# Performance work log

Measured on AMD Instinct MI355X. Metric: run time of the kernel, lower is better.

## Reference

```python
import jax, jax.numpy as jnp
import numpy as np

SR = 44100
N_FFT = 2048
N_BINS = 64
HOP = 512
POWER = 2.0
FREQ_BINS = N_FFT // 2 + 1  # 1025
BATCH = 32
LEN_AUDIO = 441000  # 10 seconds at 44.1 kHz


def _fourier_kernels():
    # Periodic (fftbins=True) Hann window, matching scipy.signal.get_window('hann', n_fft)
    n = np.arange(N_FFT)
    window = 0.5 - 0.5 * np.cos(2.0 * np.pi * n / N_FFT)
    k = np.arange(FREQ_BINS)[:, None]  # [freq_bins, 1]
    phase = 2.0 * np.pi * k * n[None, :] / N_FFT  # [freq_bins, n_fft]
    wsin = (np.sin(phase) * window[None, :]).astype(np.float32)[:, None, :]  # [F,1,n_fft]
    wcos = (np.cos(phase) * window[None, :]).astype(np.float32)[:, None, :]
    return jnp.asarray(wsin), jnp.asarray(wcos)


def setup_inputs() -> dict:
    key = jax.random.key(0)
    k1, k2 = jax.random.split(key)
    x = jax.random.normal(k1, (BATCH, 1, LEN_AUDIO), dtype=jnp.float32)
    wsin, wcos = _fourier_kernels()
    # Gammatone filterbank matrix [n_bins, freq_bins]; treated as a fixed parameter.
    gammatone_basis = jax.random.uniform(k2, (N_BINS, FREQ_BINS), dtype=jnp.float32) * 0.01
    return {"x": x, "wsin": wsin, "wcos": wcos, "gammatone_basis": gammatone_basis}


def _conv1d(x, w, stride):
    # x: [B, 1, L], w: [F, 1, K] -> [B, F, T]
    return jax.lax.conv_general_dilated(
        x, w, window_strides=(stride,), padding='VALID',
        dimension_numbers=('NCH', 'OIH', 'NCH'))


def reference(x, wsin, wcos, gammatone_basis):
    pad = N_FFT // 2
    xp = jnp.pad(x, ((0, 0), (0, 0), (pad, pad)), mode='reflect')
    s = _conv1d(xp, wsin, HOP)
    c = _conv1d(xp, wcos, HOP)
    spec = jnp.sqrt(s * s + c * c) ** POWER  # [B, F, T]
    # [n_bins, F] @ [B, F, T] -> [B, n_bins, T]
    return jnp.einsum('nf,bft->bnt', gammatone_basis, spec)
```

## Files before the change

kernel.cpp:

```cpp
#include <hip/hip_runtime.h>
#include <stdint.h>

typedef __attribute__((ext_vector_type(4))) float f32x4;
typedef __attribute__((ext_vector_type(8))) short bf16x8;
typedef __attribute__((ext_vector_type(8))) unsigned short u16x8;
typedef __attribute__((ext_vector_type(2))) unsigned int u32x2;

#define B_SZ   32
#define L_AUD  441000
#define PAD_A  1024
#define LP     443048
#define T_FR   862
#define J_TOT  27584
#define JPAD   27648
#define F_BINS 1025
#define NFFT   2048
#define NB     64
#define FPAD   1152
#define NT_J   108
#define NT_F   9
#define NWG    (NT_J * NT_F)
#define ROWB   886096

#define W2_OFF     0
#define W2_BYTES   (NT_F * 32 * 16384)
#define GB2_OFF    W2_BYTES
#define GB2_BYTES  (NB * FPAD * 2)
#define UB_OFF     (GB2_OFF + GB2_BYTES)
#define UB_BYTES   ((size_t)JPAD * 2048 * 2)
#define WS_FOLD    (UB_OFF + UB_BYTES)
#define SLAB_BYTES ((size_t)NT_F * NB * JPAD * 4)
#define WS_FOLD_SLAB (WS_FOLD + SLAB_BYTES)

#define FB_XBP_OFF   0
#define FB_XBP_BYTES (B_SZ * LP * 2)
#define FB_WBT_OFF   FB_XBP_BYTES
#define FB_WBT_BYTES (NT_F * 32 * 2 * 16384)
#define FB_GB_OFF    (FB_WBT_OFF + FB_WBT_BYTES)
#define FB_WS_NEED   (FB_GB_OFF + GB2_BYTES)
#define FB_SLAB_OFF  FB_WS_NEED
#define FB_WS_BIG    ((size_t)FB_SLAB_OFF + SLAB_BYTES)

__device__ __forceinline__ uint16_t f2bf(float f) {
  union { float f; uint32_t u; } c; c.f = f;
  uint32_t r = c.u + 0x7FFFu + ((c.u >> 16) & 1u);
  return (uint16_t)(r >> 16);
}
__device__ __forceinline__ float bf2f(uint32_t u) {
  union { uint32_t u; float f; } c; c.u = u << 16; return c.f;
}

__device__ __forceinline__ f32x4 mfma16(bf16x8 a, bf16x8 b, f32x4 c) {
  return __builtin_amdgcn_mfma_f32_16x16x32_bf16(a, b, c, 0, 0, 0);
}

#define GLD16(g, l) __builtin_amdgcn_global_load_lds( \
    (__attribute__((address_space(1))) void*)(g),     \
    (__attribute__((address_space(3))) void*)(l), 16, 0, 0)

__device__ __forceinline__ int refl(int p) {
  int s = p - PAD_A;
  s = s < 0 ? -s : s;
  s = s >= L_AUD ? (2 * L_AUD - 2 - s) : s;
  return s;
}


__global__ __launch_bounds__(256) void build_gb(const float* __restrict__ g,
                                                uint16_t* __restrict__ gb) {
  int i = blockIdx.x * 256 + threadIdx.x;
  int n = i / FPAD;
  int f = i - n * FPAD;
  gb[i] = f2bf(f < F_BINS ? g[n * F_BINS + f] : 0.0f);
}

__global__ __launch_bounds__(256) void reduce9(const float* __restrict__ slab,
                                               float* __restrict__ out) {
  int i = blockIdx.x * 256 + threadIdx.x;
  if (i >= J_TOT * NB) return;
  int b = i / (NB * T_FR);
  int rem = i - b * (NB * T_FR);
  int n = rem / T_FR;
  int t = rem - n * T_FR;
  int j = b * T_FR + t;
  float s = 0.f;
#pragma unroll
  for (int fb = 0; fb < NT_F; ++fb)
    s += slab[((size_t)fb * NB + n) * JPAD + j];
  out[i] = s;
}


__global__ __launch_bounds__(256) void build_wbt2(const float* __restrict__ wsin,
                                                  const float* __restrict__ wcos,
                                                  uint16_t* __restrict__ wbt) {
  int idx = blockIdx.x * 256 + threadIdx.x;
  int e = idx & 7;
  int s = (idx >> 3) & 7;
  int jp = (idx >> 6) & 127;
  int kkt = (idx >> 13) & 31;
  int fb = idx >> 18;
  int v = s ^ (jp & 7);
  int r = jp * 2 + (v >> 2);
  int k = (v & 3) * 8 + e;
  int plane = r >> 7;
  int f = fb * 128 + (r & 127);
  int m = kkt * 32 + k;
  float val = 0.f;
  if (f < F_BINS) {
    int mm = (m == 0) ? 1024 : m;
    val = plane ? wsin[(size_t)f * NFFT + mm] : wcos[(size_t)f * NFFT + mm];
  }
  wbt[idx] = f2bf(val);
}

__global__ __launch_bounds__(128) void build_ub(const float* __restrict__ x,
                                                uint16_t* __restrict__ ub) {
  __shared__ float xs[2048];
  int jg = blockIdx.x;
  int tid = threadIdx.x;
  uint16_t* outp = ub + (size_t)jg * 2048;
  if (jg >= J_TOT) {
    u16x8 z = (u16x8)0;
    *(u16x8*)(outp + tid * 8) = z;
    *(u16x8*)(outp + 1024 + tid * 8) = z;
    return;
  }
  int b = jg / T_FR, t = jg - b * T_FR;
  int c = t * 512;
  const float* xb = x + (size_t)b * L_AUD;
  if (t >= 2 && t <= 859) {
    const float4* src = (const float4*)(xb + c - PAD_A);
    float4* dl = (float4*)xs;
#pragma unroll
    for (int i = 0; i < 4; ++i) dl[tid * 4 + i] = src[tid * 4 + i];
  } else {
#pragma unroll
    for (int i = 0; i < 16; ++i) xs[tid * 16 + i] = xb[refl(c + tid * 16 + i)];
  }
  __syncthreads();
  int m0 = tid * 8;
  u16x8 vp, vm;
#pragma unroll
  for (int i = 0; i < 8; ++i) {
    int m = m0 + i;
    if (m == 0) { vp[i] = f2bf(xs[1024]); vm[i] = 0; }
    else {
      float a = xs[m], r = xs[2048 - m];
      vp[i] = f2bf(a + r);
      vm[i] = f2bf(a - r);
    }
  }
  *(u16x8*)(outp + m0) = vp;
  *(u16x8*)(outp + 1024 + m0) = vm;
}

template <bool USE_SLAB>
__global__ __launch_bounds__(512, 2) void gammatone_fold(
    const char* __restrict__ ub, const char* __restrict__ wbt2,
    const char* __restrict__ gb, float* __restrict__ dst) {
  __shared__ __align__(16) char smem[147456];

  const int tid = threadIdx.x;
  const int w = tid >> 6, l = tid & 63;
  const int lgrp = l >> 4, l15 = l & 15;
  const int plane = w >> 2;
  const int rw = (w >> 1) & 1;
  const int jw = w & 1;

  const int orig = blockIdx.x;
  const int xcd = orig & 7, slot = orig >> 3;
  const int q = NWG / 8, r = NWG & 7;
  const int wkid = (xcd < r ? xcd * (q + 1) : r * (q + 1) + (xcd - r) * q) + slot;
  const int jb = wkid / NT_F;
  const int fb = wkid - jb * NT_F;
  const int j0 = jb * 256;
  const int f0 = fb * 128;

  const int ssn = w >> 2, q4 = w & 3;
  const int aoff_sta = w * 2048 + l * 16;
  const int boff_sta = 16384 + ssn * 16384 + q4 * 4096 + l * 16;
  const int vsw = (l & 7) ^ (l >> 3);
  const char* bsrc[4];
#pragma unroll
  for (int i = 0; i < 4; ++i) {
    int col = j0 + q4 * 64 + i * 16 + (l >> 3) * 2 + (vsw >> 2);
    bsrc[i] = ub + (size_t)col * 4096 + ssn * 2048 + (vsw & 3) * 16;
  }
  const char* wbtA = wbt2 + (size_t)fb * 524288;

#define STAGEF(kkt, off) do {                                               \
    const char* ga_ = wbtA + (size_t)(kkt) * 16384 + aoff_sta;              \
    GLD16(ga_,        smem + (off) + aoff_sta);                             \
    GLD16(ga_ + 1024, smem + (off) + aoff_sta + 1024);                      \
    GLD16(bsrc[0] + (size_t)(kkt) * 64, smem + (off) + boff_sta);           \
    GLD16(bsrc[1] + (size_t)(kkt) * 64, smem + (off) + boff_sta + 1024);    \
    GLD16(bsrc[2] + (size_t)(kkt) * 64, smem + (off) + boff_sta + 2048);    \
    GLD16(bsrc[3] + (size_t)(kkt) * 64, smem + (off) + boff_sta + 3072);    \
  } while (0)

  const int slb = ((lgrp | ((l15 & 1) << 2)) ^ (l15 >> 1)) << 4;
  int aoff[4], bvo[8];
#pragma unroll
  for (int m = 0; m < 4; ++m)
    aoff[m] = (plane * 64 + rw * 32 + m * 8 + (l15 >> 1)) * 128 + slb;
#pragma unroll
  for (int n = 0; n < 8; ++n)
    bvo[n] = 16384 + plane * 16384 + (jw * 64 + n * 8 + (l15 >> 1)) * 128 + slb;

  STAGEF(0, 0);
  STAGEF(1, 49152);
  asm volatile("s_waitcnt vmcnt(6)" ::: "memory");
  asm volatile("s_barrier" ::: "memory");

  f32x4 acc[4][8];
#pragma unroll
  for (int m = 0; m < 4; ++m)
#pragma unroll
    for (int n = 0; n < 8; ++n) acc[m][n] = (f32x4){0.f, 0.f, 0.f, 0.f};

  unsigned b0 = 0, b1 = 49152, b2 = 98304;
  for (int kk = 0; kk < 32; ++kk) {
    bf16x8 av[4], bv[8];
#pragma unroll
    for (int m = 0; m < 4; ++m) av[m] = *(const bf16x8*)(smem + b0 + aoff[m]);
#pragma unroll
    for (int n = 0; n < 8; ++n) bv[n] = *(const bf16x8*)(smem + b0 + bvo[n]);
    if (kk < 30) STAGEF(kk + 2, b2);
    __builtin_amdgcn_s_setprio(1);
#pragma unroll
    for (int m = 0; m < 4; ++m)
#pragma unroll
      for (int n = 0; n < 8; ++n)
        acc[m][n] = mfma16(av[m], bv[n], acc[m][n]);
    __builtin_amdgcn_s_setprio(0);
    if (kk < 30)       asm volatile("s_waitcnt vmcnt(6)" ::: "memory");
    else if (kk == 30) asm volatile("s_waitcnt vmcnt(0)" ::: "memory");
    asm volatile("s_barrier" ::: "memory");
    unsigned t = b0; b0 = b1; b1 = b2; b2 = t;
  }

  __syncthreads();
  if (plane == 0) {
#pragma unroll
    for (int m = 0; m < 4; ++m) {
      int fi = rw * 64 + m * 16 + lgrp * 4;
#pragma unroll
      for (int n = 0; n < 8; ++n) {
        int j = jw * 128 + n * 16 + l15;
        f32x4 c = acc[m][n];
        uint32_t lo = (uint32_t)f2bf(c.x * c.x) |
                      ((uint32_t)f2bf(c.y * c.y) << 16);
        uint32_t hi = (uint32_t)f2bf(c.z * c.z) |
                      ((uint32_t)f2bf(c.w * c.w) << 16);
        int off = j * 256 + ((fi * 2) ^ ((j & 7) << 4));
        *(u32x2*)(smem + off) = (u32x2){lo, hi};
      }
    }
  }
  __syncthreads();
  if (plane == 1) {
#pragma unroll
    for (int m = 0; m < 4; ++m) {
      int fi = rw * 64 + m * 16 + lgrp * 4;
#pragma unroll
      for (int n = 0; n < 8; ++n) {
        int j = jw * 128 + n * 16 + l15;
        int off = j * 256 + ((fi * 2) ^ ((j & 7) << 4));
        u32x2 v = *(u32x2*)(smem + off);
        f32x4 s = acc[m][n];
        uint32_t lo = (uint32_t)f2bf(bf2f(v.x & 0xffffu) + s.x * s.x) |
                      ((uint32_t)f2bf(bf2f(v.x >> 16) + s.y * s.y) << 16);
        uint32_t hi = (uint32_t)f2bf(bf2f(v.y & 0xffffu) + s.z * s.z) |
                      ((uint32_t)f2bf(bf2f(v.y >> 16) + s.w * s.w) << 16);
        *(u32x2*)(smem + off) = (u32x2){lo, hi};
      }
    }
  }
  __syncthreads();

  f32x4 acc2[4][2];
#pragma unroll
  for (int m = 0; m < 4; ++m) {
    acc2[m][0] = (f32x4){0.f, 0.f, 0.f, 0.f};
    acc2[m][1] = (f32x4){0.f, 0.f, 0.f, 0.f};
  }
  const int jwq = w * 32;
#pragma unroll
  for (int ks = 0; ks < 4; ++ks) {
    bf16x8 gf[4], sf[2];
#pragma unroll
    for (int m2 = 0; m2 < 4; ++m2) {
      int grow = m2 * 16 + l15;
      gf[m2] = *(const bf16x8*)(gb + ((size_t)grow * FPAD + f0 + ks * 32 + lgrp * 8) * 2);
    }
#pragma unroll
    for (int nf = 0; nf < 2; ++nf) {
      int j = jwq + nf * 16 + l15;
      sf[nf] = *(const bf16x8*)(smem + j * 256 + (((ks * 32 + lgrp * 8) * 2) ^ ((j & 7) << 4)));
    }
#pragma unroll
    for (int m2 = 0; m2 < 4; ++m2)
#pragma unroll
      for (int nf = 0; nf < 2; ++nf)
        acc2[m2][nf] = mfma16(gf[m2], sf[nf], acc2[m2][nf]);
  }

#pragma unroll
  for (int nf = 0; nf < 2; ++nf) {
    int jg = j0 + jwq + nf * 16 + l15;
    if (USE_SLAB) {
      float* sl = dst + ((size_t)fb * NB) * JPAD + jg;
#pragma unroll
      for (int m2 = 0; m2 < 4; ++m2)
#pragma unroll
        for (int r2 = 0; r2 < 4; ++r2) {
          int nout = m2 * 16 + lgrp * 4 + r2;
          sl[(size_t)nout * JPAD] = acc2[m2][nf][r2];
        }
    } else if (jg < J_TOT) {
      int b = jg / T_FR;
      int t = jg - b * T_FR;
      float* ob = dst + (size_t)(b * NB) * T_FR + t;
#pragma unroll
      for (int m2 = 0; m2 < 4; ++m2)
#pragma unroll
        for (int r2 = 0; r2 < 4; ++r2) {
          int nout = m2 * 16 + lgrp * 4 + r2;
          atomicAdd(ob + (size_t)nout * T_FR, acc2[m2][nf][r2]);
        }
    }
  }
}


__global__ __launch_bounds__(256) void build_xbp(const float* __restrict__ x,
                                                 uint16_t* __restrict__ xbp) {
  int i = blockIdx.x * 256 + threadIdx.x;
  int b = i / LP;
  int p = i - b * LP;
  xbp[i] = f2bf(x[b * L_AUD + refl(p)]);
}

__global__ __launch_bounds__(256) void build_wbtf(const float* __restrict__ wsin,
                                                  const float* __restrict__ wcos,
                                                  uint16_t* __restrict__ wbt) {
  int idx = blockIdx.x * 256 + threadIdx.x;
  int e = idx & 7;
  int l = (idx >> 3) & 63;
  int s = (idx >> 9) & 1;
  int fm = (idx >> 10) & 15;
  int kkt = (idx >> 14) & 31;
  int fb = idx >> 19;
  int tr = fm * 16 + (l & 15);
  int k = kkt * 64 + s * 32 + ((l >> 4) << 3) + e;
  int plane = (tr >> 6) & 1;
  int f = fb * 128 + ((tr >> 7) << 6) + (tr & 63);
  float v = (f < F_BINS) ? (plane ? wcos[f * NFFT + k] : wsin[f * NFFT + k]) : 0.0f;
  wbt[idx] = f2bf(v);
}

__device__ __forceinline__ void load_a2(bf16x8 (&d)[2][2], const char* p) {
  d[0][0] = *(const bf16x8*)(p);
  d[0][1] = *(const bf16x8*)(p + 1024);
  d[1][0] = *(const bf16x8*)(p + 2048);
  d[1][1] = *(const bf16x8*)(p + 3072);
}
__device__ __forceinline__ void load_b4(bf16x8 (&dst)[4][2], const char* p,
                                        int k0, int k1) {
#pragma unroll
  for (int n = 0; n < 4; ++n) {
    dst[n][0] = *(const bf16x8*)(p + n * 2048 + k0);
    dst[n][1] = *(const bf16x8*)(p + n * 2048 + k1);
  }
}
__device__ __forceinline__ void mfma_pair(f32x4 (*ac)[4],
                                          const bf16x8 (&av)[2][2],
                                          const bf16x8 (&bv)[4][2]) {
#pragma unroll
  for (int m = 0; m < 2; ++m)
#pragma unroll
    for (int n = 0; n < 4; ++n) {
      ac[m][n] = mfma16(av[m][0], bv[n][0], ac[m][n]);
      ac[m][n] = mfma16(av[m][1], bv[n][1], ac[m][n]);
    }
}

template <bool USE_SLAB>
__global__ __launch_bounds__(512, 2) void gammatone_fb(
    const char* __restrict__ xbp, const char* __restrict__ wbt,
    const char* __restrict__ gb, float* __restrict__ dst) {
  __shared__ __align__(16) char smem[65536];

  const int tid = threadIdx.x;
  const int w = tid >> 6, l = tid & 63;
  const int lgrp = l >> 4, l15 = l & 15;
  const int wr = w >> 2, wc = w & 3;

  const int orig = blockIdx.y * NT_J + blockIdx.x;
  const int xcd = orig & 7, slot = orig >> 3;
  const int q = NWG / 8, r = NWG & 7;
  const int wkid = (xcd < r ? xcd * (q + 1) : r * (q + 1) + (xcd - r) * q) + slot;
  const int fb = wkid / NT_J;
  const int jb = wkid - fb * NT_J;
  const int j0 = jb * 256;
  const int f0 = fb * 128;

  const int xr = (((tid & 7) << 4)) ^ ((((tid >> 3) & 7)) << 4);
  size_t fbase[2][2];
#pragma unroll
  for (int h = 0; h < 2; ++h)
#pragma unroll
    for (int i = 0; i < 2; ++i) {
      int col = j0 + h * 128 + i * 64 + (tid >> 3);
      if (col > J_TOT - 1) col = J_TOT - 1;
      int b = col / T_FR;
      int t = col - b * T_FR;
      fbase[h][i] = (size_t)b * ROWB + (size_t)t * 1024 + (size_t)xr;
    }

#define STAGE_B2(kkt, buf) do {                                             \
    char* d0_ = smem + (buf) * 32768;                                       \
    char* d1_ = smem + (buf) * 32768 + 16384;                               \
    GLD16(xbp + fbase[0][0] + (size_t)(kkt) * 128, d0_ + w * 1024 + l * 16);\
    GLD16(xbp + fbase[0][1] + (size_t)(kkt) * 128, d0_ + 8192 + w * 1024 + l * 16);\
    GLD16(xbp + fbase[1][0] + (size_t)(kkt) * 128, d1_ + w * 1024 + l * 16);\
    GLD16(xbp + fbase[1][1] + (size_t)(kkt) * 128, d1_ + 8192 + w * 1024 + l * 16);\
  } while (0)

  const int albase = l15 * 128;
  const int xa = (l15 & 7) << 4;
  const int k0 = (lgrp * 16) ^ xa;
  const int k1 = (64 + lgrp * 16) ^ xa;
  const int jrb = (wc & 1) * 64;
  const char* Bb0 = smem + (wc >> 1) * 16384 + jrb * 128 + albase;
  const char* Bb1 = Bb0 + 32768;
  const char* wbt_a = wbt + (size_t)fb * 32 * 32768 + wr * 16384 + (size_t)l * 16;

  STAGE_B2(0, 0);
  STAGE_B2(1, 1);
  asm volatile("s_waitcnt vmcnt(0)" ::: "memory");
  __builtin_amdgcn_s_barrier();

  f32x4 acc[8][4];
#pragma unroll
  for (int m = 0; m < 8; ++m)
#pragma unroll
    for (int n = 0; n < 4; ++n) acc[m][n] = (f32x4){0.f, 0.f, 0.f, 0.f};

  bf16x8 bvA[4][2], bvB[4][2], av0[2][2], av1[2][2];
  load_b4(bvA, Bb0, k0, k1);
  load_a2(av0, wbt_a);
  asm volatile("s_waitcnt lgkmcnt(0)" ::: "memory");
  __builtin_amdgcn_s_barrier();

#define SP1 __builtin_amdgcn_s_setprio(1)
#define SP0 __builtin_amdgcn_s_setprio(0)

#define TILEFB(KK, bvC, bvN, BbN, STG, NXT) do {                            \
    const char* aT = wbt_a + (size_t)(KK) * 32768;                          \
    if (STG) STAGE_B2((KK) + 2, (KK) & 1);                                  \
    load_a2(av1, aT + 2 * 2048);                                            \
    SP1; mfma_pair(&acc[0], av0, bvC); SP0;                                 \
    load_a2(av0, aT + 4 * 2048);                                            \
    SP1; mfma_pair(&acc[2], av1, bvC); SP0;                                 \
    load_a2(av1, aT + 6 * 2048);                                            \
    if (NXT) load_b4(bvN, BbN, k0, k1);                                     \
    SP1; mfma_pair(&acc[4], av0, bvC); SP0;                                 \
    if (NXT) load_a2(av0, wbt_a + (size_t)((KK) + 1) * 32768);              \
    SP1; mfma_pair(&acc[6], av1, bvC); SP0;                                 \
    asm volatile("s_waitcnt lgkmcnt(0)" ::: "memory");                      \
    __builtin_amdgcn_s_barrier();                                           \
  } while (0)

  for (int kk = 0; kk < 30; kk += 2) {
    TILEFB(kk,     bvA, bvB, Bb1, 1, 1);
    TILEFB(kk + 1, bvB, bvA, Bb0, 1, 1);
  }
  TILEFB(30, bvA, bvB, Bb1, 0, 1);
  TILEFB(31, bvB, bvA, Bb0, 0, 0);

  __syncthreads();
#pragma unroll
  for (int m = 0; m < 4; ++m) {
    int fi = wr * 64 + m * 16 + lgrp * 4;
#pragma unroll
    for (int n = 0; n < 4; ++n) {
      int j = wc * 64 + n * 16 + l15;
      f32x4 s = acc[m][n], c = acc[m + 4][n];
      uint32_t lo = (uint32_t)f2bf(s.x * s.x + c.x * c.x) |
                    ((uint32_t)f2bf(s.y * s.y + c.y * c.y) << 16);
      uint32_t hi = (uint32_t)f2bf(s.z * s.z + c.z * c.z) |
                    ((uint32_t)f2bf(s.w * s.w + c.w * c.w) << 16);
      int off = j * 256 + ((fi * 2) ^ ((j & 7) << 4));
      *(u32x2*)(smem + off) = (u32x2){lo, hi};
    }
  }
  __syncthreads();

  f32x4 acc2[4][2];
#pragma unroll
  for (int m = 0; m < 4; ++m) {
    acc2[m][0] = (f32x4){0.f, 0.f, 0.f, 0.f};
    acc2[m][1] = (f32x4){0.f, 0.f, 0.f, 0.f};
  }
  const int jw = w * 32;
#pragma unroll
  for (int ks = 0; ks < 4; ++ks) {
    bf16x8 gf[4], sf[2];
#pragma unroll
    for (int m2 = 0; m2 < 4; ++m2) {
      int grow = m2 * 16 + l15;
      gf[m2] = *(const bf16x8*)(gb + ((size_t)grow * FPAD + f0 + ks * 32 + lgrp * 8) * 2);
    }
#pragma unroll
    for (int nf = 0; nf < 2; ++nf) {
      int j = jw + nf * 16 + l15;
      sf[nf] = *(const bf16x8*)(smem + j * 256 + (((ks * 32 + lgrp * 8) * 2) ^ ((j & 7) << 4)));
    }
#pragma unroll
    for (int m2 = 0; m2 < 4; ++m2)
#pragma unroll
      for (int nf = 0; nf < 2; ++nf)
        acc2[m2][nf] = mfma16(gf[m2], sf[nf], acc2[m2][nf]);
  }

#pragma unroll
  for (int nf = 0; nf < 2; ++nf) {
    int jg = j0 + jw + nf * 16 + l15;
    if (USE_SLAB) {
      float* sl = dst + ((size_t)fb * NB) * JPAD + jg;
#pragma unroll
      for (int m2 = 0; m2 < 4; ++m2)
#pragma unroll
        for (int r2 = 0; r2 < 4; ++r2) {
          int nout = m2 * 16 + lgrp * 4 + r2;
          sl[(size_t)nout * JPAD] = acc2[m2][nf][r2];
        }
    } else if (jg < J_TOT) {
      int b = jg / T_FR;
      int t = jg - b * T_FR;
      float* ob = dst + (size_t)(b * NB) * T_FR + t;
#pragma unroll
      for (int m2 = 0; m2 < 4; ++m2)
#pragma unroll
        for (int r2 = 0; r2 < 4; ++r2) {
          int nout = m2 * 16 + lgrp * 4 + r2;
          atomicAdd(ob + (size_t)nout * T_FR, acc2[m2][nf][r2]);
        }
    }
  }
}

extern "C" void kernel_launch(void* const* d_in, const int* in_sizes, int n_in,
                              void* d_out, int out_size, void* d_ws, size_t ws_size,
                              hipStream_t stream) {
  (void)in_sizes; (void)n_in;
  const float* x    = (const float*)d_in[0];
  const float* wsin = (const float*)d_in[1];
  const float* wcos = (const float*)d_in[2];
  const float* g    = (const float*)d_in[3];
  char* ws = (char*)d_ws;

  if (ws_size >= (size_t)WS_FOLD) {
    uint16_t* wbt2 = (uint16_t*)(ws + W2_OFF);
    uint16_t* gbp  = (uint16_t*)(ws + GB2_OFF);
    uint16_t* ub   = (uint16_t*)(ws + UB_OFF);
    build_wbt2<<<(W2_BYTES / 2) / 256, 256, 0, stream>>>(wsin, wcos, wbt2);
    build_gb<<<(NB * FPAD) / 256, 256, 0, stream>>>(g, gbp);
    build_ub<<<JPAD, 128, 0, stream>>>(x, ub);
    if (ws_size >= (size_t)WS_FOLD_SLAB) {
      float* slab = (float*)(ws + WS_FOLD);
      gammatone_fold<true><<<NWG, 512, 0, stream>>>(
          (const char*)ub, (const char*)wbt2, (const char*)gbp, slab);
      reduce9<<<(J_TOT * NB + 255) / 256, 256, 0, stream>>>(slab, (float*)d_out);
    } else {
      hipMemsetAsync(d_out, 0, (size_t)out_size * sizeof(float), stream);
      gammatone_fold<false><<<NWG, 512, 0, stream>>>(
          (const char*)ub, (const char*)wbt2, (const char*)gbp, (float*)d_out);
    }
    return;
  }

  if (ws_size < (size_t)FB_WS_NEED) return;
  uint16_t* xbp = (uint16_t*)(ws + FB_XBP_OFF);
  uint16_t* wbt = (uint16_t*)(ws + FB_WBT_OFF);
  uint16_t* gbp = (uint16_t*)(ws + FB_GB_OFF);
  build_xbp<<<(B_SZ * LP) / 256, 256, 0, stream>>>(x, xbp);
  build_wbtf<<<(FB_WBT_BYTES / 2) / 256, 256, 0, stream>>>(wsin, wcos, wbt);
  build_gb<<<(NB * FPAD) / 256, 256, 0, stream>>>(g, gbp);
  if (ws_size >= (size_t)FB_WS_BIG) {
    float* slab = (float*)(ws + FB_SLAB_OFF);
    gammatone_fb<true><<<dim3(NT_J, NT_F), 512, 0, stream>>>(
        (const char*)xbp, (const char*)wbt, (const char*)gbp, slab);
    reduce9<<<(J_TOT * NB + 255) / 256, 256, 0, stream>>>(slab, (float*)d_out);
  } else {
    hipMemsetAsync(d_out, 0, (size_t)out_size * sizeof(float), stream);
    gammatone_fb<false><<<dim3(NT_J, NT_F), 512, 0, stream>>>(
        (const char*)xbp, (const char*)wbt, (const char*)gbp, (float*)d_out);
  }
}
```

Baseline: 218.4 us.

## Pre-swizzle operands into MFMA fragment layout and load directly to registers

The A (windowed Fourier) and B (folded audio frame) operands are now stored in global memory already arranged in the MFMA fragment order. The main GEMM loop can then read them straight into registers with double-buffered global loads, with no LDS staging and no barriers. The j-tile is halved to 128, which doubles the workgroup count and shrinks shared memory to 32KB. In exchange, each workgroup loses the LDS reuse of operands across waves, so more global/L2 traffic is needed, and latency hiding relies only on the register prefetch.

```diff
diff --git a/kernel.cpp b/kernel.cpp
--- a/kernel.cpp
+++ b/kernel.cpp
@@ -17,9 +17,9 @@
 #define NFFT   2048
 #define NB     64
 #define FPAD   1152
-#define NT_J   108
 #define NT_F   9
-#define NWG    (NT_J * NT_F)
+#define NT_J2  216
+#define NWG2   (NT_J2 * NT_F)
 #define ROWB   886096
 
 #define W2_OFF     0
@@ -40,6 +40,8 @@
 #define FB_WS_NEED   (FB_GB_OFF + GB2_BYTES)
 #define FB_SLAB_OFF  FB_WS_NEED
 #define FB_WS_BIG    ((size_t)FB_SLAB_OFF + SLAB_BYTES)
+#define FB_NT_J      108
+#define FB_NWG       (FB_NT_J * NT_F)
 
 __device__ __forceinline__ uint16_t f2bf(float f) {
   union { float f; uint32_t u; } c; c.f = f;
@@ -91,39 +93,39 @@
 }
 
 
-__global__ __launch_bounds__(256) void build_wbt2(const float* __restrict__ wsin,
+__global__ __launch_bounds__(256) void build_wbt3(const float* __restrict__ wsin,
                                                   const float* __restrict__ wcos,
                                                   uint16_t* __restrict__ wbt) {
   int idx = blockIdx.x * 256 + threadIdx.x;
   int e = idx & 7;
-  int s = (idx >> 3) & 7;
-  int jp = (idx >> 6) & 127;
+  int lane = (idx >> 3) & 63;
+  int fm = (idx >> 9) & 15;
   int kkt = (idx >> 13) & 31;
   int fb = idx >> 18;
-  int v = s ^ (jp & 7);
-  int r = jp * 2 + (v >> 2);
-  int k = (v & 3) * 8 + e;
-  int plane = r >> 7;
-  int f = fb * 128 + (r & 127);
-  int m = kkt * 32 + k;
+  int row = fm * 16 + (lane & 15);
+  int k = kkt * 32 + ((lane >> 4) << 3) + e;
+  int plane = row >> 7;
+  int f = fb * 128 + (row & 127);
   float val = 0.f;
   if (f < F_BINS) {
-    int mm = (m == 0) ? 1024 : m;
+    int mm = (k == 0) ? 1024 : k;
     val = plane ? wsin[(size_t)f * NFFT + mm] : wcos[(size_t)f * NFFT + mm];
   }
   wbt[idx] = f2bf(val);
 }
 
-__global__ __launch_bounds__(128) void build_ub(const float* __restrict__ x,
-                                                uint16_t* __restrict__ ub) {
+__global__ __launch_bounds__(128) void build_ubf(const float* __restrict__ x,
+                                                 uint16_t* __restrict__ ub) {
   __shared__ float xs[2048];
   int jg = blockIdx.x;
   int tid = threadIdx.x;
-  uint16_t* outp = ub + (size_t)jg * 2048;
+  int m0 = tid * 8;
+  size_t basef = (((size_t)(jg >> 4) * 32 + (m0 >> 5)) * 2) * 1024 +
+                 (size_t)((((m0 >> 3) & 3) * 16 + (jg & 15)) * 16);
   if (jg >= J_TOT) {
     u16x8 z = (u16x8)0;
-    *(u16x8*)(outp + tid * 8) = z;
-    *(u16x8*)(outp + 1024 + tid * 8) = z;
+    *(u16x8*)((char*)ub + basef) = z;
+    *(u16x8*)((char*)ub + basef + 1024) = z;
     return;
   }
   int b = jg / T_FR, t = jg - b * T_FR;
@@ -139,7 +141,6 @@
     for (int i = 0; i < 16; ++i) xs[tid * 16 + i] = xb[refl(c + tid * 16 + i)];
   }
   __syncthreads();
-  int m0 = tid * 8;
   u16x8 vp, vm;
 #pragma unroll
   for (int i = 0; i < 8; ++i) {
@@ -151,15 +152,18 @@
       vm[i] = f2bf(a - r);
     }
   }
-  *(u16x8*)(outp + m0) = vp;
-  *(u16x8*)(outp + 1024 + m0) = vm;
-}
+  *(u16x8*)((char*)ub + basef) = vp;
+  *(u16x8*)((char*)ub + basef + 1024) = vm;
+}
+
+#define SP1 __builtin_amdgcn_s_setprio(1)
+#define SP0 __builtin_amdgcn_s_setprio(0)
 
 template <bool USE_SLAB>
-__global__ __launch_bounds__(512, 2) void gammatone_fold(
-    const char* __restrict__ ub, const char* __restrict__ wbt2,
+__global__ __launch_bounds__(512, 2) void gammatone_fold2(
+    const char* __restrict__ ubf, const char* __restrict__ wbt3,
     const char* __restrict__ gb, float* __restrict__ dst) {
-  __shared__ __align__(16) char smem[147456];
+  __shared__ __align__(16) char smem[32768];
 
   const int tid = threadIdx.x;
   const int w = tid >> 6, l = tid & 63;
@@ -169,76 +173,57 @@
   const int jw = w & 1;
 
   const int orig = blockIdx.x;
-  const int xcd = orig & 7, slot = orig >> 3;
-  const int q = NWG / 8, r = NWG & 7;
-  const int wkid = (xcd < r ? xcd * (q + 1) : r * (q + 1) + (xcd - r) * q) + slot;
+  const int wkid = (orig & 7) * 243 + (orig >> 3);
   const int jb = wkid / NT_F;
   const int fb = wkid - jb * NT_F;
-  const int j0 = jb * 256;
+  const int j0 = jb * 128;
   const int f0 = fb * 128;
 
-  const int ssn = w >> 2, q4 = w & 3;
-  const int aoff_sta = w * 2048 + l * 16;
-  const int boff_sta = 16384 + ssn * 16384 + q4 * 4096 + l * 16;
-  const int vsw = (l & 7) ^ (l >> 3);
-  const char* bsrc[4];
-#pragma unroll
-  for (int i = 0; i < 4; ++i) {
-    int col = j0 + q4 * 64 + i * 16 + (l >> 3) * 2 + (vsw >> 2);
-    bsrc[i] = ub + (size_t)col * 4096 + ssn * 2048 + (vsw & 3) * 16;
-  }
-  const char* wbtA = wbt2 + (size_t)fb * 524288;
-
-#define STAGEF(kkt, off) do {                                               \
-    const char* ga_ = wbtA + (size_t)(kkt) * 16384 + aoff_sta;              \
-    GLD16(ga_,        smem + (off) + aoff_sta);                             \
-    GLD16(ga_ + 1024, smem + (off) + aoff_sta + 1024);                      \
-    GLD16(bsrc[0] + (size_t)(kkt) * 64, smem + (off) + boff_sta);           \
-    GLD16(bsrc[1] + (size_t)(kkt) * 64, smem + (off) + boff_sta + 1024);    \
-    GLD16(bsrc[2] + (size_t)(kkt) * 64, smem + (off) + boff_sta + 2048);    \
-    GLD16(bsrc[3] + (size_t)(kkt) * 64, smem + (off) + boff_sta + 3072);    \
+  const char* aB = wbt3 + (((size_t)fb * 32) * 16 + plane * 8 + rw * 4) * 1024
+                        + (size_t)l * 16;
+  const char* bB = ubf + (((size_t)(jb * 8 + jw * 4) * 32) * 2 + plane) * 1024
+                       + (size_t)l * 16;
+
+#define LOADT(kkt, av_, bv_) do {                                           \
+    const char* a_ = aB + (size_t)(kkt) * 16384;                            \
+    const char* b_ = bB + (size_t)(kkt) * 2048;                             \
+    av_[0] = *(const bf16x8*)(a_);                                          \
+    av_[1] = *(const bf16x8*)(a_ + 1024);                                   \
+    av_[2] = *(const bf16x8*)(a_ + 2048);                                   \
+    av_[3] = *(const bf16x8*)(a_ + 3072);                                   \
+    bv_[0] = *(const bf16x8*)(b_);                                          \
+    bv_[1] = *(const bf16x8*)(b_ + 65536);                                  \
+    bv_[2] = *(const bf16x8*)(b_ + 131072);                                 \
+    bv_[3] = *(const bf16x8*)(b_ + 196608);                                 \
   } while (0)
 
-  const int slb = ((lgrp | ((l15 & 1) << 2)) ^ (l15 >> 1)) << 4;
-  int aoff[4], bvo[8];
+  f32x4 acc[4][4];
 #pragma unroll
   for (int m = 0; m < 4; ++m)
-    aoff[m] = (plane * 64 + rw * 32 + m * 8 + (l15 >> 1)) * 128 + slb;
-#pragma unroll
-  for (int n = 0; n < 8; ++n)
-    bvo[n] = 16384 + plane * 16384 + (jw * 64 + n * 8 + (l15 >> 1)) * 128 + slb;
-
-  STAGEF(0, 0);
-  STAGEF(1, 49152);
-  asm volatile("s_waitcnt vmcnt(6)" ::: "memory");
-  asm volatile("s_barrier" ::: "memory");
-
-  f32x4 acc[4][8];
-#pragma unroll
-  for (int m = 0; m < 4; ++m)
-#pragma unroll
-    for (int n = 0; n < 8; ++n) acc[m][n] = (f32x4){0.f, 0.f, 0.f, 0.f};
-
-  unsigned b0 = 0, b1 = 49152, b2 = 98304;
-  for (int kk = 0; kk < 32; ++kk) {
-    bf16x8 av[4], bv[8];
-#pragma unroll
-    for (int m = 0; m < 4; ++m) av[m] = *(const bf16x8*)(smem + b0 + aoff[m]);
-#pragma unroll
-    for (int n = 0; n < 8; ++n) bv[n] = *(const bf16x8*)(smem + b0 + bvo[n]);
-    if (kk < 30) STAGEF(kk + 2, b2);
-    __builtin_amdgcn_s_setprio(1);
-#pragma unroll
-    for (int m = 0; m < 4; ++m)
-#pragma unroll
-      for (int n = 0; n < 8; ++n)
-        acc[m][n] = mfma16(av[m], bv[n], acc[m][n]);
-    __builtin_amdgcn_s_setprio(0);
-    if (kk < 30)       asm volatile("s_waitcnt vmcnt(6)" ::: "memory");
-    else if (kk == 30) asm volatile("s_waitcnt vmcnt(0)" ::: "memory");
-    asm volatile("s_barrier" ::: "memory");
-    unsigned t = b0; b0 = b1; b1 = b2; b2 = t;
-  }
+#pragma unroll
+    for (int n = 0; n < 4; ++n) acc[m][n] = (f32x4){0.f, 0.f, 0.f, 0.f};
+
+#define MM(av_, bv_) do {                                                   \
+    SP1;                                                                    \
+    _Pragma("unroll")                                                       \
+    for (int m = 0; m < 4; ++m)                                             \
+      _Pragma("unroll")                                                     \
+      for (int n = 0; n < 4; ++n)                                           \
+        acc[m][n] = mfma16(av_[m], bv_[n], acc[m][n]);                      \
+    SP0;                                                                    \
+  } while (0)
+
+  bf16x8 avA[4], bvA[4], avB[4], bvB[4];
+  LOADT(0, avA, bvA);
+  LOADT(1, avB, bvB);
+  for (int kk = 0; kk < 30; kk += 2) {
+    MM(avA, bvA);
+    LOADT(kk + 2, avA, bvA);
+    MM(avB, bvB);
+    LOADT(kk + 3, avB, bvB);
+  }
+  MM(avA, bvA);
+  MM(avB, bvB);
 
   __syncthreads();
   if (plane == 0) {
@@ -246,8 +231,8 @@
     for (int m = 0; m < 4; ++m) {
       int fi = rw * 64 + m * 16 + lgrp * 4;
 #pragma unroll
-      for (int n = 0; n < 8; ++n) {
-        int j = jw * 128 + n * 16 + l15;
+      for (int n = 0; n < 4; ++n) {
+        int j = jw * 64 + n * 16 + l15;
         f32x4 c = acc[m][n];
         uint32_t lo = (uint32_t)f2bf(c.x * c.x) |
                       ((uint32_t)f2bf(c.y * c.y) << 16);
@@ -264,8 +249,8 @@
     for (int m = 0; m < 4; ++m) {
       int fi = rw * 64 + m * 16 + lgrp * 4;
 #pragma unroll
-      for (int n = 0; n < 8; ++n) {
-        int j = jw * 128 + n * 16 + l15;
+      for (int n = 0; n < 4; ++n) {
+        int j = jw * 64 + n * 16 + l15;
         int off = j * 256 + ((fi * 2) ^ ((j & 7) << 4));
         u32x2 v = *(u32x2*)(smem + off);
         f32x4 s = acc[m][n];
@@ -279,36 +264,29 @@
   }
   __syncthreads();
 
-  f32x4 acc2[4][2];
-#pragma unroll
-  for (int m = 0; m < 4; ++m) {
-    acc2[m][0] = (f32x4){0.f, 0.f, 0.f, 0.f};
-    acc2[m][1] = (f32x4){0.f, 0.f, 0.f, 0.f};
-  }
-  const int jwq = w * 32;
+  f32x4 acc2[4];
+#pragma unroll
+  for (int m = 0; m < 4; ++m) acc2[m] = (f32x4){0.f, 0.f, 0.f, 0.f};
+  const int jwq = w * 16;
 #pragma unroll
   for (int ks = 0; ks < 4; ++ks) {
-    bf16x8 gf[4], sf[2];
+    bf16x8 gf[4], sf;
 #pragma unroll
     for (int m2 = 0; m2 < 4; ++m2) {
       int grow = m2 * 16 + l15;
       gf[m2] = *(const bf16x8*)(gb + ((size_t)grow * FPAD + f0 + ks * 32 + lgrp * 8) * 2);
     }
-#pragma unroll
-    for (int nf = 0; nf < 2; ++nf) {
-      int j = jwq + nf * 16 + l15;
-      sf[nf] = *(const bf16x8*)(smem + j * 256 + (((ks * 32 + lgrp * 8) * 2) ^ ((j & 7) << 4)));
+    {
+      int j = jwq + l15;
+      sf = *(const bf16x8*)(smem + j * 256 + (((ks * 32 + lgrp * 8) * 2) ^ ((j & 7) << 4)));
     }
 #pragma unroll
     for (int m2 = 0; m2 < 4; ++m2)
-#pragma unroll
-      for (int nf = 0; nf < 2; ++nf)
-        acc2[m2][nf] = mfma16(gf[m2], sf[nf], acc2[m2][nf]);
-  }
-
-#pragma unroll
-  for (int nf = 0; nf < 2; ++nf) {
-    int jg = j0 + jwq + nf * 16 + l15;
+      acc2[m2] = mfma16(gf[m2], sf, acc2[m2]);
+  }
+
+  {
+    int jg = j0 + jwq + l15;
     if (USE_SLAB) {
       float* sl = dst + ((size_t)fb * NB) * JPAD + jg;
 #pragma unroll
@@ -316,7 +294,7 @@
 #pragma unroll
         for (int r2 = 0; r2 < 4; ++r2) {
           int nout = m2 * 16 + lgrp * 4 + r2;
-          sl[(size_t)nout * JPAD] = acc2[m2][nf][r2];
+          sl[(size_t)nout * JPAD] = acc2[m2][r2];
         }
     } else if (jg < J_TOT) {
       int b = jg / T_FR;
@@ -327,7 +305,7 @@
 #pragma unroll
         for (int r2 = 0; r2 < 4; ++r2) {
           int nout = m2 * 16 + lgrp * 4 + r2;
-          atomicAdd(ob + (size_t)nout * T_FR, acc2[m2][nf][r2]);
+          atomicAdd(ob + (size_t)nout * T_FR, acc2[m2][r2]);
         }
     }
   }
@@ -397,12 +375,12 @@
   const int lgrp = l >> 4, l15 = l & 15;
   const int wr = w >> 2, wc = w & 3;
 
-  const int orig = blockIdx.y * NT_J + blockIdx.x;
+  const int orig = blockIdx.y * FB_NT_J + blockIdx.x;
   const int xcd = orig & 7, slot = orig >> 3;
-  const int q = NWG / 8, r = NWG & 7;
+  const int q = FB_NWG / 8, r = FB_NWG & 7;
   const int wkid = (xcd < r ? xcd * (q + 1) : r * (q + 1) + (xcd - r) * q) + slot;
-  const int fb = wkid / NT_J;
-  const int jb = wkid - fb * NT_J;
+  const int fb = wkid / FB_NT_J;
+  const int jb = wkid - fb * FB_NT_J;
   const int j0 = jb * 256;
   const int f0 = fb * 128;
 
@@ -453,9 +431,6 @@
   load_a2(av0, wbt_a);
   asm volatile("s_waitcnt lgkmcnt(0)" ::: "memory");
   __builtin_amdgcn_s_barrier();
-
-#define SP1 __builtin_amdgcn_s_setprio(1)
-#define SP0 __builtin_amdgcn_s_setprio(0)
 
 #define TILEFB(KK, bvC, bvN, BbN, STG, NXT) do {                            \
     const char* aT = wbt_a + (size_t)(KK) * 32768;                          \
@@ -504,7 +479,7 @@
     acc2[m][0] = (f32x4){0.f, 0.f, 0.f, 0.f};
     acc2[m][1] = (f32x4){0.f, 0.f, 0.f, 0.f};
   }
-  const int jw = w * 32;
+  const int jw2 = w * 32;
 #pragma unroll
   for (int ks = 0; ks < 4; ++ks) {
     bf16x8 gf[4], sf[2];
@@ -515,7 +490,7 @@
     }
 #pragma unroll
     for (int nf = 0; nf < 2; ++nf) {
-      int j = jw + nf * 16 + l15;
+      int j = jw2 + nf * 16 + l15;
       sf[nf] = *(const bf16x8*)(smem + j * 256 + (((ks * 32 + lgrp * 8) * 2) ^ ((j & 7) << 4)));
     }
 #pragma unroll
@@ -527,7 +502,7 @@
 
 #pragma unroll
   for (int nf = 0; nf < 2; ++nf) {
-    int jg = j0 + jw + nf * 16 + l15;
+    int jg = j0 + jw2 + nf * 16 + l15;
     if (USE_SLAB) {
       float* sl = dst + ((size_t)fb * NB) * JPAD + jg;
 #pragma unroll
@@ -563,21 +538,21 @@
   char* ws = (char*)d_ws;
 
   if (ws_size >= (size_t)WS_FOLD) {
-    uint16_t* wbt2 = (uint16_t*)(ws + W2_OFF);
+    uint16_t* wbt3 = (uint16_t*)(ws + W2_OFF);
     uint16_t* gbp  = (uint16_t*)(ws + GB2_OFF);
-    uint16_t* ub   = (uint16_t*)(ws + UB_OFF);
-    build_wbt2<<<(W2_BYTES / 2) / 256, 256, 0, stream>>>(wsin, wcos, wbt2);
+    uint16_t* ubf  = (uint16_t*)(ws + UB_OFF);
+    build_wbt3<<<(W2_BYTES / 2) / 256, 256, 0, stream>>>(wsin, wcos, wbt3);
     build_gb<<<(NB * FPAD) / 256, 256, 0, stream>>>(g, gbp);
-    build_ub<<<JPAD, 128, 0, stream>>>(x, ub);
+    build_ubf<<<JPAD, 128, 0, stream>>>(x, ubf);
     if (ws_size >= (size_t)WS_FOLD_SLAB) {
       float* slab = (float*)(ws + WS_FOLD);
-      gammatone_fold<true><<<NWG, 512, 0, stream>>>(
-          (const char*)ub, (const char*)wbt2, (const char*)gbp, slab);
+      gammatone_fold2<true><<<NWG2, 512, 0, stream>>>(
+          (const char*)ubf, (const char*)wbt3, (const char*)gbp, slab);
       reduce9<<<(J_TOT * NB + 255) / 256, 256, 0, stream>>>(slab, (float*)d_out);
     } else {
       hipMemsetAsync(d_out, 0, (size_t)out_size * sizeof(float), stream);
-      gammatone_fold<false><<<NWG, 512, 0, stream>>>(
-          (const char*)ub, (const char*)wbt2, (const char*)gbp, (float*)d_out);
+      gammatone_fold2<false><<<NWG2, 512, 0, stream>>>(
+          (const char*)ubf, (const char*)wbt3, (const char*)gbp, (float*)d_out);
     }
     return;
   }
@@ -591,12 +566,12 @@
   build_gb<<<(NB * FPAD) / 256, 256, 0, stream>>>(g, gbp);
   if (ws_size >= (size_t)FB_WS_BIG) {
     float* slab = (float*)(ws + FB_SLAB_OFF);
-    gammatone_fb<true><<<dim3(NT_J, NT_F), 512, 0, stream>>>(
+    gammatone_fb<true><<<dim3(FB_NT_J, NT_F), 512, 0, stream>>>(
         (const char*)xbp, (const char*)wbt, (const char*)gbp, slab);
     reduce9<<<(J_TOT * NB + 255) / 256, 256, 0, stream>>>(slab, (float*)d_out);
   } else {
     hipMemsetAsync(d_out, 0, (size_t)out_size * sizeof(float), stream);
-    gammatone_fb<false><<<dim3(NT_J, NT_F), 512, 0, stream>>>(
+    gammatone_fb<false><<<dim3(FB_NT_J, NT_F), 512, 0, stream>>>(
         (const char*)xbp, (const char*)wbt, (const char*)gbp, (float*)d_out);
   }
 }
```

Measured after the change: 317.6 us. +45.4%, slower.
